# Kernel optimization log

Measured on AMD Instinct MI355X. Metric: run time of the kernel, lower is better.

The kernel has to match this reference:

```python
import jax, jax.numpy as jnp
import numpy as np

B, Z, H, W = 4, 128, 256, 256
L = 64  # number of pseudo-labels (0 = ignore)
SIM_COEFF, STD_COEFF, COV_COEFF = 1.0, 1.0, 1.0
EPS_STD = 1e-4


def setup_inputs() -> dict:
    key = jax.random.key(0)
    k1, k2, k3, k4 = jax.random.split(key, 4)
    pred = jax.random.normal(k1, (B, Z, H, W), jnp.float32)
    pred_mv = jax.random.normal(k2, (B, Z, H, W), jnp.float32)
    gt = jax.random.randint(k3, (B, H, W), 0, L, jnp.int32)
    fov_mask = jax.random.uniform(k4, (B, H, W)) < 0.8
    return {"pred": pred, "pred_mv": pred_mv, "gt": gt, "fov_mask": fov_mask}


def _std_loss(z, w):
    # torch.var(dim=0) is unbiased (n-1); masked version via weights w in {0,1}
    n = w.sum()
    mean = (z * w[:, None]).sum(0) / n
    var = (((z - mean) ** 2) * w[:, None]).sum(0) / (n - 1.0)
    std = jnp.sqrt(var + EPS_STD)
    return jnp.mean(jax.nn.relu(1.0 - std))


def _cov_loss(z, w):
    n = w.sum()
    mean = (z * w[:, None]).sum(0) / n
    zc = (z - mean) * w[:, None]  # masked-out rows contribute zero
    cov = (zc.T @ zc) / (n - 1.0)  # [Z, Z]
    off_sq = (cov ** 2).sum() - (jnp.diagonal(cov) ** 2).sum()
    return off_sq / Z


def reference(pred, pred_mv, gt, fov_mask):
    mask = fov_mask & (gt != 0)                     # [B,H,W]
    P = H * W
    wf = mask.astype(pred.dtype).reshape(B * P)     # 0/1 weights, flattened
    a = pred.transpose(0, 2, 3, 1).reshape(B * P, Z)      # anchor feats
    m = pred_mv.transpose(0, 2, 3, 1).reshape(B * P, Z)   # multiview feats

    # ---- sim loss: per-batch, per-label pairwise masked MSE via segment sums ----
    # sum_{l} sum_{i,j in l} ||a_i - m_j||^2 = sum_l [ n_l*(S|a|^2 + S|m|^2) - 2 (Sa).(Sm) ]
    seg = (gt.reshape(B, P) + jnp.arange(B, dtype=gt.dtype)[:, None] * L).reshape(-1)
    n_l = jax.ops.segment_sum(wf, seg, num_segments=B * L)                    # [B*L]
    sumA = jax.ops.segment_sum(a * wf[:, None], seg, num_segments=B * L)      # [B*L,Z]
    sumM = jax.ops.segment_sum(m * wf[:, None], seg, num_segments=B * L)
    sqA = jax.ops.segment_sum((a ** 2).sum(-1) * wf, seg, num_segments=B * L)  # [B*L]
    sqM = jax.ops.segment_sum((m ** 2).sum(-1) * wf, seg, num_segments=B * L)
    total = (n_l * (sqA + sqM)).sum() - 2.0 * (sumA * sumM).sum()
    count = (n_l ** 2).sum()  # = sum over batches of mask_exp.sum()
    sim_loss = total / count

    # ---- std (variance) loss over all masked points of each view ----
    std_loss = _std_loss(a, wf) + _std_loss(m, wf)

    # ---- covariance loss ----
    cov_loss = _cov_loss(a, wf) + _cov_loss(m, wf)

    return SIM_COEFF * sim_loss + STD_COEFF * std_loss + COV_COEFF * cov_loss
```

## Files before the change

kernel.cpp:

```cpp
#include <hip/hip_runtime.h>
#include <stdint.h>

#define B_DIM 4
#define Z_DIM 128
#define L_DIM 64
#define P_DIM 65536
#define CHUNK 128

typedef short sh8  __attribute__((ext_vector_type(8)));
typedef short sh4v __attribute__((ext_vector_type(4)));
typedef float f32x4 __attribute__((ext_vector_type(4)));

__device__ __forceinline__ unsigned short bfc(float x) {
  uint32_t u = __float_as_uint(x);
  u += 0x7FFFu + ((u >> 16) & 1u);
  return (unsigned short)(u >> 16);
}

__device__ __forceinline__ int swz(int row, int k) {
  return (row * CHUNK + k) ^ ((row & 7) << 3);
}

__global__ __launch_bounds__(256, 2)
void pass1_k(const float* __restrict__ pred, const float* __restrict__ predmv,
             const int* __restrict__ gt, const uint8_t* __restrict__ fov,
             float* __restrict__ gpart, float* __restrict__ spart,
             float* __restrict__ qpart, int NB, int nchunks) {
  const int cb = blockIdx.x, b = blockIdx.y, view = blockIdx.z;
  const float* __restrict__ src = (view ? predmv : pred) + (size_t)b * Z_DIM * P_DIM;
  const int* __restrict__ gtb = gt + (size_t)b * P_DIM;
  const uint8_t* __restrict__ fovb = fov + (size_t)b * P_DIM;
  const int t = threadIdx.x;
  const int wid = t >> 6, lane = t & 63;

  __shared__ __align__(16) unsigned short tile[Z_DIM * CHUNK];
  __shared__ __align__(16) unsigned short oh[L_DIM * CHUNK];
  __shared__ float sqpx[CHUNK];
  __shared__ float sqseg[L_DIM];
  __shared__ int   lab[CHUNK];
  __shared__ float warr[CHUNK];

  if (t < L_DIM) sqseg[t] = 0.f;

  f32x4 accg[2][8];
  f32x4 accs[8];
  const f32x4 zero4 = {0.f, 0.f, 0.f, 0.f};
#pragma unroll
  for (int i = 0; i < 2; ++i)
#pragma unroll
    for (int j = 0; j < 8; ++j) accg[i][j] = zero4;
#pragma unroll
  for (int j = 0; j < 8; ++j) accs[j] = zero4;

  const int pb0 = cb * (P_DIM / NB);
  const int zr  = t >> 5;
  const int px4 = (t & 31) << 2;

  for (int c = 0; c < nchunks; ++c) {
    const int pb = pb0 + c * CHUNK;
    __syncthreads();
    {
      uint32_t* ohw = (uint32_t*)oh;
#pragma unroll
      for (int i = 0; i < (L_DIM * CHUNK / 2) / 256; ++i) ohw[t + i * 256] = 0u;
    }
    if (t < CHUNK) {
      const int g = gtb[pb + t];
      const int w = (fovb[pb + t] != 0 && g != 0) ? 1 : 0;
      lab[t]  = g & 63;
      warr[t] = (float)w;
      sqpx[t] = 0.f;
    }
    __syncthreads();
    if (t < CHUNK && warr[t] != 0.f)
      oh[swz(lab[t], t)] = 0x3F80;

    float s0 = 0.f, s1 = 0.f, s2 = 0.f, s3 = 0.f;
    const float w0 = warr[px4], w1 = warr[px4 + 1], w2 = warr[px4 + 2], w3 = warr[px4 + 3];
#pragma unroll
    for (int r = 0; r < 16; ++r) {
      const int z = zr + r * 8;
      const float4 v = *(const float4*)(src + (size_t)z * P_DIM + pb + px4);
      const float a0 = v.x * w0, a1 = v.y * w1, a2 = v.z * w2, a3 = v.w * w3;
      s0 += a0 * a0; s1 += a1 * a1; s2 += a2 * a2; s3 += a3 * a3;
      sh4v pk;
      pk.x = (short)bfc(a0); pk.y = (short)bfc(a1);
      pk.z = (short)bfc(a2); pk.w = (short)bfc(a3);
      *(sh4v*)&tile[swz(z, px4)] = pk;
    }
    atomicAdd(&sqpx[px4 + 0], s0); atomicAdd(&sqpx[px4 + 1], s1);
    atomicAdd(&sqpx[px4 + 2], s2); atomicAdd(&sqpx[px4 + 3], s3);
    __syncthreads();
    if (t < CHUNK) atomicAdd(&sqseg[lab[t]], sqpx[t]);

#pragma unroll
    for (int ks = 0; ks < 4; ++ks) {
      const int kb = ks * 32 + ((lane >> 4) << 3);
      sh8 fz[8], fa[2], ohf;
#pragma unroll
      for (int zt = 0; zt < 8; ++zt)
        fz[zt] = *(const sh8*)&tile[swz(zt * 16 + (lane & 15), kb)];
#pragma unroll
      for (int i = 0; i < 2; ++i)
        fa[i] = *(const sh8*)&tile[swz((2 * wid + i) * 16 + (lane & 15), kb)];
      ohf = *(const sh8*)&oh[swz(wid * 16 + (lane & 15), kb)];
#pragma unroll
      for (int i = 0; i < 2; ++i)
#pragma unroll
        for (int tj = 0; tj < 8; ++tj)
          accg[i][tj] = __builtin_amdgcn_mfma_f32_16x16x32_bf16(fa[i], fz[tj], accg[i][tj], 0, 0, 0);
#pragma unroll
      for (int zt = 0; zt < 8; ++zt)
        accs[zt] = __builtin_amdgcn_mfma_f32_16x16x32_bf16(ohf, fz[zt], accs[zt], 0, 0, 0);
    }
  }
  __syncthreads();

  const size_t slot = (size_t)(view * 4 + b) * NB + cb;
  float* gp = gpart + slot * (36 * 256);
#pragma unroll
  for (int i = 0; i < 2; ++i) {
    const int ti = 2 * wid + i;
#pragma unroll
    for (int tj = 0; tj < 8; ++tj) {
      if (tj >= ti) {
        const int lin = ti * 8 - (ti * (ti - 1)) / 2 + (tj - ti);
        float* dst = gp + lin * 256 + (lane >> 4) * 64 + (lane & 15);
#pragma unroll
        for (int r = 0; r < 4; ++r) dst[r * 16] = accg[i][tj][r];
      }
    }
  }
  float* sp = spart + slot * (32 * 256) + wid * (8 * 256);
#pragma unroll
  for (int zt = 0; zt < 8; ++zt) {
    float* dst = sp + zt * 256 + (lane >> 4) * 64 + (lane & 15);
#pragma unroll
    for (int r = 0; r < 4; ++r) dst[r * 16] = accs[zt][r];
  }
  if (t < L_DIM) qpart[slot * 64 + t] = sqseg[t];
}

__global__ void nl_k(const int* __restrict__ gt, const uint8_t* __restrict__ fov,
                     int* __restrict__ nl) {
  __shared__ int cnt[L_DIM];
  const int t = threadIdx.x;
  if (t < L_DIM) cnt[t] = 0;
  __syncthreads();
  const int b = blockIdx.x >> 4;
  const int base = b * P_DIM + (blockIdx.x & 15) * 4096;
  for (int i = 0; i < 16; ++i) {
    const int p = base + i * 256 + t;
    const int g = gt[p];
    if (fov[p] != 0 && g != 0) atomicAdd(&cnt[g & 63], 1);
  }
  __syncthreads();
  if (t < L_DIM) atomicAdd(&nl[b * L_DIM + t], cnt[t]);
}

__global__ void reduce_k(const float* __restrict__ gpart, const float* __restrict__ spart,
                         const float* __restrict__ qpart, float* __restrict__ gred,
                         float* __restrict__ sred, float* __restrict__ qred, int NB) {
  int id = blockIdx.x * blockDim.x + threadIdx.x;
  const int GE = 2 * 36 * 256, SE = 2 * 4 * 32 * 256, QE = 2 * 4 * 64;
  if (id < GE) {
    const int v = id / (36 * 256), e = id % (36 * 256);
    const float* p = gpart + (size_t)v * 4 * NB * (36 * 256) + e;
    float acc = 0.f;
    for (int s = 0; s < 4 * NB; ++s) acc += p[(size_t)s * (36 * 256)];
    gred[id] = acc;
  } else if ((id -= GE) < SE) {
    const int vb = id / (32 * 256);
    const float* p = spart + (size_t)vb * NB * (32 * 256) + (id % (32 * 256));
    float acc = 0.f;
    for (int s = 0; s < NB; ++s) acc += p[(size_t)s * (32 * 256)];
    sred[id] = acc;
  } else if ((id -= SE) < QE) {
    const int vb = id / 64;
    const float* p = qpart + (size_t)vb * NB * 64 + (id % 64);
    float acc = 0.f;
    for (int s = 0; s < NB; ++s) acc += p[(size_t)s * 64];
    qred[id] = acc;
  }
}

__global__ void finalize_k(const float* __restrict__ gred, const float* __restrict__ sred,
                           const float* __restrict__ qred, const int* __restrict__ nl,
                           float* __restrict__ out) {
  const int t = threadIdx.x;
  __shared__ double red[256];
  __shared__ double mu[2][128];
  __shared__ double scal[8];
  __shared__ int tti[36], ttj[36];
  if (t == 0) {
    int idx = 0;
    for (int ti = 0; ti < 8; ++ti)
      for (int tj = ti; tj < 8; ++tj) { tti[idx] = ti; ttj[idx] = tj; ++idx; }
  }
  const double nlv = (double)nl[t];

  red[t] = nlv;
  __syncthreads();
  for (int s = 128; s > 0; s >>= 1) { if (t < s) red[t] += red[t + s]; __syncthreads(); }
  if (t == 0) scal[0] = red[0];
  __syncthreads();
  const double n = scal[0];

  red[t] = nlv * nlv;
  __syncthreads();
  for (int s = 128; s > 0; s >>= 1) { if (t < s) red[t] += red[t + s]; __syncthreads(); }
  if (t == 0) scal[1] = red[0];
  __syncthreads();

  {
    const int b = t >> 6, l = t & 63;
    const double sqa = (double)qred[(0 * 4 + b) * 64 + l];
    const double sqm = (double)qred[(1 * 4 + b) * 64 + l];
    double dot = 0.0;
    for (int z = 0; z < 128; ++z) {
      const int e = ((l & 15) << 4) + (z & 15);
      const int ia = (((0 * 4 + b) * 4 + (l >> 4)) * 8 + (z >> 4)) * 256 + e;
      const int im = (((1 * 4 + b) * 4 + (l >> 4)) * 8 + (z >> 4)) * 256 + e;
      dot += (double)sred[ia] * (double)sred[im];
    }
    red[t] = nlv * (sqa + sqm) - 2.0 * dot;
  }
  __syncthreads();
  for (int s = 128; s > 0; s >>= 1) { if (t < s) red[t] += red[t + s]; __syncthreads(); }
  if (t == 0) scal[2] = red[0];
  __syncthreads();

  {
    const int v = t >> 7, z = t & 127;
    double s = 0.0;
    for (int b = 0; b < 4; ++b)
      for (int l = 0; l < 64; ++l)
        s += (double)sred[(((v * 4 + b) * 4 + (l >> 4)) * 8 + (z >> 4)) * 256 + ((l & 15) << 4) + (z & 15)];
    mu[v][z] = s / n;
  }
  __syncthreads();

  {
    const int v = t >> 7, z = t & 127;
    const int zt = z >> 4;
    const int lin = zt * 8 - (zt * (zt - 1)) / 2;
    const double gd = (double)gred[v * 9216 + lin * 256 + (z & 15) * 17];
    const double var = (gd - n * mu[v][z] * mu[v][z]) / (n - 1.0);
    const double sd = sqrt(var + 1e-4);
    const double rr = 1.0 - sd;
    red[t] = rr > 0.0 ? rr : 0.0;
  }
  __syncthreads();
  for (int s = 64; s > 0; s >>= 1) { if ((t & 127) < s) red[t] += red[t + s]; __syncthreads(); }
  if (t == 0)   scal[3] = red[0] / 128.0;
  if (t == 128) scal[4] = red[128] / 128.0;
  __syncthreads();

  for (int v = 0; v < 2; ++v) {
    double acc = 0.0;
    for (int idx = t; idx < 9216; idx += 256) {
      const int lin = idx >> 8, e = idx & 255;
      const int i = tti[lin] * 16 + (e >> 4), j = ttj[lin] * 16 + (e & 15);
      if (i < j) {
        const double g = (double)gred[v * 9216 + idx];
        const double cv = (g - n * mu[v][i] * mu[v][j]) / (n - 1.0);
        acc += 2.0 * cv * cv;
      }
    }
    red[t] = acc;
    __syncthreads();
    for (int s = 128; s > 0; s >>= 1) { if (t < s) red[t] += red[t + s]; __syncthreads(); }
    if (t == 0) scal[5 + v] = red[0] / 128.0;
    __syncthreads();
  }

  if (t == 0)
    out[0] = (float)(scal[2] / scal[1] + scal[3] + scal[4] + scal[5] + scal[6]);
}

extern "C" void kernel_launch(void* const* d_in, const int* in_sizes, int n_in,
                              void* d_out, int out_size, void* d_ws, size_t ws_size,
                              hipStream_t stream) {
  const float*  pred   = (const float*)d_in[0];
  const float*  predmv = (const float*)d_in[1];
  const int*    gt     = (const int*)d_in[2];
  const uint8_t* fov   = (const uint8_t*)d_in[3];
  float* out = (float*)d_out;

  int NB = 64;
  const size_t per_slot = 36 * 256 + 32 * 256 + 64;
  const size_t reserved = (size_t)(2 * 36 * 256 + 2 * 4 * 32 * 256 + 2 * 4 * 64 + 256) * 4 + 1024;
  while (NB > 1 && (size_t)8 * NB * per_slot * 4 + reserved > ws_size) NB >>= 1;

  float* ws    = (float*)d_ws;
  float* gpart = ws;
  float* spart = gpart + (size_t)8 * NB * (36 * 256);
  float* qpart = spart + (size_t)8 * NB * (32 * 256);
  float* gred  = qpart + (size_t)8 * NB * 64;
  float* sred  = gred + 2 * 36 * 256;
  float* qred  = sred + 2 * 4 * 32 * 256;
  int*   nl    = (int*)(qred + 2 * 4 * 64);

  hipMemsetAsync(nl, 0, 256 * sizeof(int), stream);
  nl_k<<<dim3(64), dim3(256), 0, stream>>>(gt, fov, nl);
  pass1_k<<<dim3(NB, 4, 2), dim3(256), 0, stream>>>(pred, predmv, gt, fov,
                                                    gpart, spart, qpart, NB, 512 / NB);
  const int tot = 2 * 36 * 256 + 2 * 4 * 32 * 256 + 2 * 4 * 64;
  reduce_k<<<dim3((tot + 255) / 256), dim3(256), 0, stream>>>(gpart, spart, qpart,
                                                              gred, sred, qred, NB);
  finalize_k<<<dim3(1), dim3(256), 0, stream>>>(gred, sred, qred, nl, out);
}
```

Baseline: 435.7 us.

## Prefetch next chunk into registers and fold label counting into main pass

Loads the next chunk's features, labels and FOV mask into registers while the current chunk's MFMA work runs, so global loads overlap with compute. Label counts and the per-segment squared sums are now accumulated directly from the per-thread registers. This removes the separate counting kernel and its memset, plus the shared sqpx/lab/warr staging and one barrier stage. In exchange it holds 16 float4 prefetch registers per thread, which raises VGPR pressure at two blocks per CU, and it adds a barrier around building the one-hot tile.

Result: slower. 472.3 us (+8.4%).

```diff
diff --git a/kernel.cpp b/kernel.cpp
--- a/kernel.cpp
+++ b/kernel.cpp
@@ -35,12 +35,10 @@
 
   __shared__ __align__(16) unsigned short tile[Z_DIM * CHUNK];
   __shared__ __align__(16) unsigned short oh[L_DIM * CHUNK];
-  __shared__ float sqpx[CHUNK];
   __shared__ float sqseg[L_DIM];
-  __shared__ int   lab[CHUNK];
-  __shared__ float warr[CHUNK];
-
-  if (t < L_DIM) sqseg[t] = 0.f;
+  __shared__ int   cnt[L_DIM];
+
+  if (t < L_DIM) { sqseg[t] = 0.f; cnt[t] = 0; }
 
   f32x4 accg[2][8];
   f32x4 accs[8];
@@ -56,42 +54,72 @@
   const int zr  = t >> 5;
   const int px4 = (t & 31) << 2;
 
+  float4 rv[16];
+  int4   g4;  uchar4 f4;
+  {
+    const int pb = pb0;
+    g4 = *(const int4*)(gtb + pb + px4);
+    f4 = *(const uchar4*)(fovb + pb + px4);
+#pragma unroll
+    for (int r = 0; r < 16; ++r)
+      rv[r] = *(const float4*)(src + (size_t)(zr + r * 8) * P_DIM + pb + px4);
+  }
+
   for (int c = 0; c < nchunks; ++c) {
-    const int pb = pb0 + c * CHUNK;
-    __syncthreads();
-    {
-      uint32_t* ohw = (uint32_t*)oh;
-#pragma unroll
-      for (int i = 0; i < (L_DIM * CHUNK / 2) / 256; ++i) ohw[t + i * 256] = 0u;
-    }
-    if (t < CHUNK) {
-      const int g = gtb[pb + t];
-      const int w = (fovb[pb + t] != 0 && g != 0) ? 1 : 0;
-      lab[t]  = g & 63;
-      warr[t] = (float)w;
-      sqpx[t] = 0.f;
-    }
-    __syncthreads();
-    if (t < CHUNK && warr[t] != 0.f)
-      oh[swz(lab[t], t)] = 0x3F80;
+    __syncthreads();
+
+    const float w0 = (f4.x != 0 && g4.x != 0) ? 1.f : 0.f;
+    const float w1 = (f4.y != 0 && g4.y != 0) ? 1.f : 0.f;
+    const float w2 = (f4.z != 0 && g4.z != 0) ? 1.f : 0.f;
+    const float w3 = (f4.w != 0 && g4.w != 0) ? 1.f : 0.f;
 
     float s0 = 0.f, s1 = 0.f, s2 = 0.f, s3 = 0.f;
-    const float w0 = warr[px4], w1 = warr[px4 + 1], w2 = warr[px4 + 2], w3 = warr[px4 + 3];
 #pragma unroll
     for (int r = 0; r < 16; ++r) {
       const int z = zr + r * 8;
-      const float4 v = *(const float4*)(src + (size_t)z * P_DIM + pb + px4);
-      const float a0 = v.x * w0, a1 = v.y * w1, a2 = v.z * w2, a3 = v.w * w3;
+      const float a0 = rv[r].x * w0, a1 = rv[r].y * w1;
+      const float a2 = rv[r].z * w2, a3 = rv[r].w * w3;
       s0 += a0 * a0; s1 += a1 * a1; s2 += a2 * a2; s3 += a3 * a3;
       sh4v pk;
       pk.x = (short)bfc(a0); pk.y = (short)bfc(a1);
       pk.z = (short)bfc(a2); pk.w = (short)bfc(a3);
       *(sh4v*)&tile[swz(z, px4)] = pk;
     }
-    atomicAdd(&sqpx[px4 + 0], s0); atomicAdd(&sqpx[px4 + 1], s1);
-    atomicAdd(&sqpx[px4 + 2], s2); atomicAdd(&sqpx[px4 + 3], s3);
-    __syncthreads();
-    if (t < CHUNK) atomicAdd(&sqseg[lab[t]], sqpx[t]);
+    {
+      uint4* ohv = (uint4*)oh;
+      uint4 z4; z4.x = 0u; z4.y = 0u; z4.z = 0u; z4.w = 0u;
+#pragma unroll
+      for (int i = 0; i < 4; ++i) ohv[t + i * 256] = z4;
+    }
+    if (w0 != 0.f) atomicAdd(&sqseg[g4.x & 63], s0);
+    if (w1 != 0.f) atomicAdd(&sqseg[g4.y & 63], s1);
+    if (w2 != 0.f) atomicAdd(&sqseg[g4.z & 63], s2);
+    if (w3 != 0.f) atomicAdd(&sqseg[g4.w & 63], s3);
+    if (zr == 0) {
+      if (w0 != 0.f) atomicAdd(&cnt[g4.x & 63], 1);
+      if (w1 != 0.f) atomicAdd(&cnt[g4.y & 63], 1);
+      if (w2 != 0.f) atomicAdd(&cnt[g4.z & 63], 1);
+      if (w3 != 0.f) atomicAdd(&cnt[g4.w & 63], 1);
+    }
+
+    int4 g4n = g4; uchar4 f4n = f4;
+    if (c + 1 < nchunks) {
+      const int pbn = pb0 + (c + 1) * CHUNK;
+      g4n = *(const int4*)(gtb + pbn + px4);
+      f4n = *(const uchar4*)(fovb + pbn + px4);
+#pragma unroll
+      for (int r = 0; r < 16; ++r)
+        rv[r] = *(const float4*)(src + (size_t)(zr + r * 8) * P_DIM + pbn + px4);
+    }
+
+    __syncthreads();
+    if (zr == 0) {
+      if (w0 != 0.f) oh[swz(g4.x & 63, px4 + 0)] = 0x3F80;
+      if (w1 != 0.f) oh[swz(g4.y & 63, px4 + 1)] = 0x3F80;
+      if (w2 != 0.f) oh[swz(g4.z & 63, px4 + 2)] = 0x3F80;
+      if (w3 != 0.f) oh[swz(g4.w & 63, px4 + 3)] = 0x3F80;
+    }
+    __syncthreads();
 
 #pragma unroll
     for (int ks = 0; ks < 4; ++ks) {
@@ -113,6 +141,8 @@
       for (int zt = 0; zt < 8; ++zt)
         accs[zt] = __builtin_amdgcn_mfma_f32_16x16x32_bf16(ohf, fz[zt], accs[zt], 0, 0, 0);
     }
+
+    g4 = g4n; f4 = f4n;
   }
   __syncthreads();
 
@@ -138,31 +168,17 @@
 #pragma unroll
     for (int r = 0; r < 4; ++r) dst[r * 16] = accs[zt][r];
   }
-  if (t < L_DIM) qpart[slot * 64 + t] = sqseg[t];
-}
-
-__global__ void nl_k(const int* __restrict__ gt, const uint8_t* __restrict__ fov,
-                     int* __restrict__ nl) {
-  __shared__ int cnt[L_DIM];
-  const int t = threadIdx.x;
-  if (t < L_DIM) cnt[t] = 0;
-  __syncthreads();
-  const int b = blockIdx.x >> 4;
-  const int base = b * P_DIM + (blockIdx.x & 15) * 4096;
-  for (int i = 0; i < 16; ++i) {
-    const int p = base + i * 256 + t;
-    const int g = gt[p];
-    if (fov[p] != 0 && g != 0) atomicAdd(&cnt[g & 63], 1);
-  }
-  __syncthreads();
-  if (t < L_DIM) atomicAdd(&nl[b * L_DIM + t], cnt[t]);
+  if (t < L_DIM) {
+    qpart[slot * 128 + t]          = sqseg[t];
+    qpart[slot * 128 + L_DIM + t]  = (float)cnt[t];
+  }
 }
 
 __global__ void reduce_k(const float* __restrict__ gpart, const float* __restrict__ spart,
                          const float* __restrict__ qpart, float* __restrict__ gred,
                          float* __restrict__ sred, float* __restrict__ qred, int NB) {
   int id = blockIdx.x * blockDim.x + threadIdx.x;
-  const int GE = 2 * 36 * 256, SE = 2 * 4 * 32 * 256, QE = 2 * 4 * 64;
+  const int GE = 2 * 36 * 256, SE = 2 * 4 * 32 * 256, QE = 2 * 4 * 128;
   if (id < GE) {
     const int v = id / (36 * 256), e = id % (36 * 256);
     const float* p = gpart + (size_t)v * 4 * NB * (36 * 256) + e;
@@ -176,17 +192,16 @@
     for (int s = 0; s < NB; ++s) acc += p[(size_t)s * (32 * 256)];
     sred[id] = acc;
   } else if ((id -= SE) < QE) {
-    const int vb = id / 64;
-    const float* p = qpart + (size_t)vb * NB * 64 + (id % 64);
+    const int vb = id >> 7;
+    const float* p = qpart + (size_t)vb * NB * 128 + (id & 127);
     float acc = 0.f;
-    for (int s = 0; s < NB; ++s) acc += p[(size_t)s * 64];
+    for (int s = 0; s < NB; ++s) acc += p[(size_t)s * 128];
     qred[id] = acc;
   }
 }
 
 __global__ void finalize_k(const float* __restrict__ gred, const float* __restrict__ sred,
-                           const float* __restrict__ qred, const int* __restrict__ nl,
-                           float* __restrict__ out) {
+                           const float* __restrict__ qred, float* __restrict__ out) {
   const int t = threadIdx.x;
   __shared__ double red[256];
   __shared__ double mu[2][128];
@@ -197,7 +212,8 @@
     for (int ti = 0; ti < 8; ++ti)
       for (int tj = ti; tj < 8; ++tj) { tti[idx] = ti; ttj[idx] = tj; ++idx; }
   }
-  const double nlv = (double)nl[t];
+  const int bb = t >> 6, ll = t & 63;
+  const double nlv = (double)qred[bb * 128 + 64 + ll];
 
   red[t] = nlv;
   __syncthreads();
@@ -213,14 +229,13 @@
   __syncthreads();
 
   {
-    const int b = t >> 6, l = t & 63;
-    const double sqa = (double)qred[(0 * 4 + b) * 64 + l];
-    const double sqm = (double)qred[(1 * 4 + b) * 64 + l];
+    const double sqa = (double)qred[(0 * 4 + bb) * 128 + ll];
+    const double sqm = (double)qred[(1 * 4 + bb) * 128 + ll];
     double dot = 0.0;
     for (int z = 0; z < 128; ++z) {
-      const int e = ((l & 15) << 4) + (z & 15);
-      const int ia = (((0 * 4 + b) * 4 + (l >> 4)) * 8 + (z >> 4)) * 256 + e;
-      const int im = (((1 * 4 + b) * 4 + (l >> 4)) * 8 + (z >> 4)) * 256 + e;
+      const int e = ((ll & 15) << 4) + (z & 15);
+      const int ia = (((0 * 4 + bb) * 4 + (ll >> 4)) * 8 + (z >> 4)) * 256 + e;
+      const int im = (((1 * 4 + bb) * 4 + (ll >> 4)) * 8 + (z >> 4)) * 256 + e;
       dot += (double)sred[ia] * (double)sred[im];
     }
     red[t] = nlv * (sqa + sqm) - 2.0 * dot;
@@ -288,25 +303,22 @@
   float* out = (float*)d_out;
 
   int NB = 64;
-  const size_t per_slot = 36 * 256 + 32 * 256 + 64;
-  const size_t reserved = (size_t)(2 * 36 * 256 + 2 * 4 * 32 * 256 + 2 * 4 * 64 + 256) * 4 + 1024;
+  const size_t per_slot = 36 * 256 + 32 * 256 + 128;
+  const size_t reserved = (size_t)(2 * 36 * 256 + 2 * 4 * 32 * 256 + 2 * 4 * 128) * 4 + 1024;
   while (NB > 1 && (size_t)8 * NB * per_slot * 4 + reserved > ws_size) NB >>= 1;
 
   float* ws    = (float*)d_ws;
   float* gpart = ws;
   float* spart = gpart + (size_t)8 * NB * (36 * 256);
   float* qpart = spart + (size_t)8 * NB * (32 * 256);
-  float* gred  = qpart + (size_t)8 * NB * 64;
+  float* gred  = qpart + (size_t)8 * NB * 128;
   float* sred  = gred + 2 * 36 * 256;
   float* qred  = sred + 2 * 4 * 32 * 256;
-  int*   nl    = (int*)(qred + 2 * 4 * 64);
-
-  hipMemsetAsync(nl, 0, 256 * sizeof(int), stream);
-  nl_k<<<dim3(64), dim3(256), 0, stream>>>(gt, fov, nl);
+
   pass1_k<<<dim3(NB, 4, 2), dim3(256), 0, stream>>>(pred, predmv, gt, fov,
                                                     gpart, spart, qpart, NB, 512 / NB);
-  const int tot = 2 * 36 * 256 + 2 * 4 * 32 * 256 + 2 * 4 * 64;
+  const int tot = 2 * 36 * 256 + 2 * 4 * 32 * 256 + 2 * 4 * 128;
   reduce_k<<<dim3((tot + 255) / 256), dim3(256), 0, stream>>>(gpart, spart, qpart,
                                                               gred, sred, qred, NB);
-  finalize_k<<<dim3(1), dim3(256), 0, stream>>>(gred, sred, qred, nl, out);
-}
+  finalize_k<<<dim3(1), dim3(256), 0, stream>>>(gred, sred, qred, out);
+}
```
